# Kernel tuning notes

Measured on AMD Instinct MI355X. Metric: run time of the kernel, lower is better.

Reference implementation:

```python
import jax, jax.numpy as jnp
import numpy as np

# Config (lite version of KimiK2): 2 layers, dim 2048, 16 heads x 128, MLA latent rank 512,
# 4 experts / top-2, SwiGLU inter dim 1024, vocab 32000, batch 2, seq 1024.
DEPTH, DIM, H, HD, R, DFF, E, TOPK, V, B, S = 2, 2048, 16, 128, 512, 1024, 4, 2, 32000, 2, 1024
EPS = 1e-6


def rmsnorm(x, w):
    var = jnp.mean(jnp.square(x), axis=-1, keepdims=True)
    return x * jax.lax.rsqrt(var + EPS) * w


def setup_inputs() -> dict:
    key = jax.random.key(0)
    ks = jax.random.split(key, 16)
    sd = 0.02
    d = {
        'x_tokens': jax.random.randint(ks[0], (B, S), 0, V),
        'emb': jax.random.normal(ks[1], (V, DIM), jnp.float32) * sd,
        'embed_norm_w': jnp.ones((DIM,), jnp.float32),
        # per-layer stacked params (leading axis DEPTH)
        'norm_w': jnp.ones((DEPTH, DIM), jnp.float32),
        'Wq': jax.random.normal(ks[2], (DEPTH, DIM, H * HD), jnp.float32) * sd,
        'Wdkv': jax.random.normal(ks[3], (DEPTH, DIM, R), jnp.float32) * sd,
        'Wuk': jax.random.normal(ks[4], (DEPTH, R, H * HD), jnp.float32) * sd,
        'Wuv': jax.random.normal(ks[5], (DEPTH, R, H * HD), jnp.float32) * sd,
        'Wo': jax.random.normal(ks[6], (DEPTH, H * HD, DIM), jnp.float32) * sd,
        'Wg': jax.random.normal(ks[7], (DEPTH, DIM, E), jnp.float32) * sd,
        'W1': jax.random.normal(ks[8], (DEPTH, E, DIM, DFF), jnp.float32) * sd,
        'W3': jax.random.normal(ks[9], (DEPTH, E, DIM, DFF), jnp.float32) * sd,
        'W2': jax.random.normal(ks[10], (DEPTH, E, DFF, DIM), jnp.float32) * sd,
        'head_norm_w': jnp.ones((DIM,), jnp.float32),
        'head_W': jax.random.normal(ks[11], (DIM, V), jnp.float32) * sd,
        'head_b': jnp.zeros((V,), jnp.float32),
    }
    return d


def mla(x, Wq, Wdkv, Wuk, Wuv, Wo):
    # Multi-head latent attention: queries from x, K/V from a low-rank latent c.
    Bq, Sq, _ = x.shape
    q = (x @ Wq).reshape(Bq, Sq, H, HD)
    c = x @ Wdkv                                   # [B,S,R] compressed KV latent
    k = (c @ Wuk).reshape(Bq, Sq, H, HD)
    v = (c @ Wuv).reshape(Bq, Sq, H, HD)
    scores = jnp.einsum('bqhd,bkhd->bhqk', q, k) / jnp.sqrt(jnp.float32(HD))
    a = jax.nn.softmax(scores, axis=-1)            # block never passes a mask -> full attention
    o = jnp.einsum('bhqk,bkhd->bqhd', a, v).reshape(Bq, Sq, H * HD)
    return o @ Wo


def moe(x, Wg, W1, W3, W2):
    # x: [B,S,D] -> flatten tokens. Dense-over-experts (E=4) with top-k masked gates.
    Bq, Sq, Dq = x.shape
    xt = x.reshape(Bq * Sq, Dq)                    # [T,D]
    gate = jax.nn.softmax(xt @ Wg, axis=-1)        # [T,E]
    topv, topi = jax.lax.top_k(gate, TOPK)
    topv = topv / jnp.sum(topv, axis=-1, keepdims=True)
    gw = jnp.zeros_like(gate).at[jnp.arange(xt.shape[0])[:, None], topi].set(topv)  # [T,E]
    h = jnp.einsum('td,edf->etf', xt, W1)
    g = jnp.einsum('td,edf->etf', xt, W3)
    eo = jnp.einsum('etf,efd->etd', jax.nn.silu(h) * g, W2)
    out = jnp.einsum('etd,te->td', eo, gw)
    return out.reshape(Bq, Sq, Dq)


def reference(x_tokens, emb, embed_norm_w, norm_w, Wq, Wdkv, Wuk, Wuv, Wo, Wg, W1, W3, W2, head_norm_w, head_W, head_b):
    h = emb[x_tokens]
    h = rmsnorm(h, embed_norm_w)

    def layer(h, p):
        nw, wq, wdkv, wuk, wuv, wo, wg, w1, w3, w2 = p
        h = h + mla(rmsnorm(h, nw), wq, wdkv, wuk, wuv, wo)
        # NOTE: same norm weight reused pre-MoE, as in the torch module
        h = h + moe(rmsnorm(h, nw), wg, w1, w3, w2)
        return h, None

    h, _ = jax.lax.scan(layer, h, (norm_w, Wq, Wdkv, Wuk, Wuv, Wo, Wg, W1, W3, W2))
    return rmsnorm(h, head_norm_w) @ head_W + head_b
```

## Files before the change

### kernel.cpp

```cpp
#include <hip/hip_runtime.h>
#include <hip/hip_bf16.h>

typedef __hip_bfloat16 bf16;
typedef __bf16 bf16x8 __attribute__((ext_vector_type(8)));
typedef float f32x4 __attribute__((ext_vector_type(4)));
typedef unsigned short u16;
typedef unsigned int u32;

static constexpr int TOKS = 2048, DM = 2048, RL = 512, DF = 1024, SQ = 1024, NV = 32000;
static constexpr long PL_X  = (long)TOKS * DM;
static constexpr long PL_C  = (long)TOKS * RL;
static constexpr long PL_VT = 2l * 16 * 128 * 1024;
static constexpr long M4 = 4l * 1024 * 1024;
static constexpr long M2 = 2l * 1024 * 1024;

__device__ __forceinline__ float b2f(bf16 x){ return __bfloat162float(x); }
__device__ __forceinline__ bf16  f2b(float x){ return __float2bfloat16(x); }
__device__ __forceinline__ void split1(float x, u16& h, u16& l){
  bf16 hb = f2b(x);
  float r = x - b2f(hb);
  bf16 lb = f2b(r);
  h = *(u16*)&hb; l = *(u16*)&lb;
}

__device__ __forceinline__ float block_red(float v, int op){
  __shared__ float red[4];
  const int lane = threadIdx.x & 63, wv = threadIdx.x >> 6;
  #pragma unroll
  for (int off = 32; off > 0; off >>= 1){
    float o = __shfl_down(v, off, 64);
    v = op ? fmaxf(v, o) : v + o;
  }
  __syncthreads();
  if (lane == 0) red[wv] = v;
  __syncthreads();
  float r = red[0];
  #pragma unroll
  for (int i = 1; i < 4; ++i) r = op ? fmaxf(r, red[i]) : r + red[i];
  return r;
}

__global__ __launch_bounds__(256)
void embed_norm_k(const int* __restrict__ toks, const float* __restrict__ emb,
                  const float* __restrict__ w, float* __restrict__ h){
  const int t = blockIdx.x;
  const long tok = toks[t];
  const int base = threadIdx.x * 8;
  const float* ep = emb + tok * (long)DM + base;
  float4 va = *(const float4*)ep, vb = *(const float4*)(ep + 4);
  float v[8] = {va.x, va.y, va.z, va.w, vb.x, vb.y, vb.z, vb.w};
  float ss = 0.f;
  #pragma unroll
  for (int i = 0; i < 8; ++i) ss += v[i]*v[i];
  ss = block_red(ss, 0);
  const float inv = rsqrtf(ss / DM + 1e-6f);
  float4 wa = *(const float4*)(w + base), wb4 = *(const float4*)(w + base + 4);
  float wv[8] = {wa.x, wa.y, wa.z, wa.w, wb4.x, wb4.y, wb4.z, wb4.w};
  float* hp = h + (long)t * DM + base;
  #pragma unroll
  for (int i = 0; i < 8; ++i) hp[i] = v[i] * inv * wv[i];
}

__global__ __launch_bounds__(256)
void rmsnorm_planes_k(const float* __restrict__ h, const float* __restrict__ w,
                      u16* __restrict__ hi, u16* __restrict__ lo){
  const int t = blockIdx.x;
  const int base = threadIdx.x * 8;
  const float* hp = h + (long)t * DM + base;
  float4 va = *(const float4*)hp, vb = *(const float4*)(hp + 4);
  float v[8] = {va.x, va.y, va.z, va.w, vb.x, vb.y, vb.z, vb.w};
  float ss = 0.f;
  #pragma unroll
  for (int i = 0; i < 8; ++i) ss += v[i]*v[i];
  ss = block_red(ss, 0);
  const float inv = rsqrtf(ss / DM + 1e-6f);
  float4 wa = *(const float4*)(w + base), wb4 = *(const float4*)(w + base + 4);
  float wv[8] = {wa.x, wa.y, wa.z, wa.w, wb4.x, wb4.y, wb4.z, wb4.w};
  u16 hvv[8], lvv[8];
  #pragma unroll
  for (int i = 0; i < 8; ++i) split1(v[i] * inv * wv[i], hvv[i], lvv[i]);
  *(int4*)(hi + (long)t * DM + base) = *(const int4*)hvv;
  *(int4*)(lo + (long)t * DM + base) = *(const int4*)lvv;
}

__global__ __launch_bounds__(256)
void gate_k(const float* __restrict__ h, const float* __restrict__ nw,
            const float* __restrict__ Wg, float* __restrict__ gw){
  const int t = blockIdx.x;
  const int base = threadIdx.x * 8;
  const float* hp = h + (long)t * DM + base;
  float4 va = *(const float4*)hp, vb = *(const float4*)(hp + 4);
  float v[8] = {va.x, va.y, va.z, va.w, vb.x, vb.y, vb.z, vb.w};
  float ss = 0.f;
  #pragma unroll
  for (int i = 0; i < 8; ++i) ss += v[i]*v[i];
  ss = block_red(ss, 0);
  const float inv = rsqrtf(ss / DM + 1e-6f);
  float a[4] = {0.f, 0.f, 0.f, 0.f};
  #pragma unroll
  for (int i = 0; i < 8; ++i){
    const float xv = v[i] * inv * nw[base + i];
    #pragma unroll
    for (int e = 0; e < 4; ++e) a[e] += xv * Wg[(base + i)*4 + e];
  }
  #pragma unroll
  for (int e = 0; e < 4; ++e) a[e] = block_red(a[e], 0);
  if (threadIdx.x == 0){
    int i1 = 0;
    for (int e = 1; e < 4; ++e) if (a[e] > a[i1]) i1 = e;
    int i2 = -1;
    for (int e = 0; e < 4; ++e){ if (e == i1) continue; if (i2 < 0 || a[e] > a[i2]) i2 = e; }
    float g[4];
    const float m = fmaxf(fmaxf(a[0], a[1]), fmaxf(a[2], a[3]));
    float s = 0.f;
    for (int e = 0; e < 4; ++e){ g[e] = __expf(a[e] - m); s += g[e]; }
    for (int e = 0; e < 4; ++e) g[e] /= s;
    const float ns = g[i1] + g[i2];
    float* op = gw + (long)t * 4;
    op[0] = 0.f; op[1] = 0.f; op[2] = 0.f; op[3] = 0.f;
    op[i1] = g[i1] / ns; op[i2] = g[i2] / ns;
  }
}

__global__ __launch_bounds__(256)
void softmax_pack_k(float* __restrict__ pf){
  const long row = blockIdx.x;
  const float* pr = pf + row * SQ;
  const int base = threadIdx.x * 4;
  float4 v4 = *(const float4*)(pr + base);
  float v[4] = {v4.x, v4.y, v4.z, v4.w};
  float m = fmaxf(fmaxf(v[0], v[1]), fmaxf(v[2], v[3]));
  m = block_red(m, 1);
  float s = 0.f;
  #pragma unroll
  for (int i = 0; i < 4; ++i){ v[i] = __expf(v[i] - m); s += v[i]; }
  s = block_red(s, 0);
  const float inv = 1.f / s;
  u16 hv[4], lv[4];
  #pragma unroll
  for (int i = 0; i < 4; ++i) split1(v[i] * inv, hv[i], lv[i]);
  u16* out = (u16*)pf + row * 2048;
  *(int2*)(out + base) = *(const int2*)hv;
  *(int2*)(out + 1024 + base) = *(const int2*)lv;
}

__global__ __launch_bounds__(256)
void swiglu_pack_k(float* __restrict__ h1, const float* __restrict__ h3){
  const int t = threadIdx.x;
  const long r = (long)blockIdx.x * 2 + (t >> 7);
  const int col = (t & 127) * 8;
  const float* p1 = h1 + r * 1024 + col;
  const float* p3 = h3 + r * 1024 + col;
  float4 a0 = *(const float4*)p1, a1 = *(const float4*)(p1 + 4);
  float4 b0 = *(const float4*)p3, b1 = *(const float4*)(p3 + 4);
  float a[8] = {a0.x, a0.y, a0.z, a0.w, a1.x, a1.y, a1.z, a1.w};
  float b[8] = {b0.x, b0.y, b0.z, b0.w, b1.x, b1.y, b1.z, b1.w};
  u16 hv[8], lv[8];
  #pragma unroll
  for (int j = 0; j < 8; ++j){
    const float y = (a[j] / (1.f + __expf(-a[j]))) * b[j];
    split1(y, hv[j], lv[j]);
  }
  __syncthreads();
  u16* out = (u16*)h1 + r * 2048;
  *(int4*)(out + col) = *(const int4*)hv;
  *(int4*)(out + 1024 + col) = *(const int4*)lv;
}

__global__ __launch_bounds__(256)
void swiglu_bk(bf16* __restrict__ h1, const bf16* __restrict__ h3){
  const long i = ((long)blockIdx.x * 256 + threadIdx.x) * 8;
  union { int4 i4; bf16 b[8]; } x, y;
  x.i4 = *(const int4*)(h1 + i);
  y.i4 = *(const int4*)(h3 + i);
  #pragma unroll
  for (int j = 0; j < 8; ++j){
    const float a = b2f(x.b[j]);
    const float b = b2f(y.b[j]);
    x.b[j] = f2b((a / (1.f + __expf(-a))) * b);
  }
  *(int4*)(h1 + i) = x.i4;
}

__global__ __launch_bounds__(256)
void tsplit_k(const float* __restrict__ in, long inz, int ldin,
              u16* __restrict__ oh, u16* __restrict__ ol, long outz, int ldout, int ntx){
  __shared__ u16 lh[64][72], ll[64][72];
  const int z = blockIdx.z;
  in += (long)z * inz; oh += (long)z * outz; ol += (long)z * outz;
  const int bx = blockIdx.x % ntx, by = blockIdx.x / ntx;
  const int k0 = by * 64, n0 = bx * 64;
  const int t = threadIdx.x;
  {
    const int r = t >> 2, cb = (t & 3) * 16;
    const float* ip = in + (long)(k0 + r) * ldin + n0 + cb;
    #pragma unroll
    for (int i = 0; i < 16; i += 4){
      float4 v = *(const float4*)(ip + i);
      float a[4] = {v.x, v.y, v.z, v.w};
      #pragma unroll
      for (int j = 0; j < 4; ++j){
        u16 hv, lv; split1(a[j], hv, lv);
        lh[r][cb + i + j] = hv; ll[r][cb + i + j] = lv;
      }
    }
  }
  __syncthreads();
  {
    const int n = t >> 2, kb = (t & 3) * 16;
    u16 hv[16], lv[16];
    #pragma unroll
    for (int i = 0; i < 16; ++i){ hv[i] = lh[kb + i][n]; lv[i] = ll[kb + i][n]; }
    u16* po = oh + (long)(n0 + n) * ldout + k0 + kb;
    u16* pl = ol + (long)(n0 + n) * ldout + k0 + kb;
    *(int4*)po = *(const int4*)hv; *(int4*)(po + 8) = *(const int4*)(hv + 8);
    *(int4*)pl = *(const int4*)lv; *(int4*)(pl + 8) = *(const int4*)(lv + 8);
  }
}

__global__ __launch_bounds__(256)
void tconv_k(const float* __restrict__ in, long inz, int ldin,
             bf16* __restrict__ out, long outz, int ldout, int ntx){
  __shared__ u16 lh[64][72];
  const int z = blockIdx.z;
  in += (long)z * inz; out += (long)z * outz;
  const int bx = blockIdx.x % ntx, by = blockIdx.x / ntx;
  const int k0 = by * 64, n0 = bx * 64;
  const int t = threadIdx.x;
  {
    const int r = t >> 2, cb = (t & 3) * 16;
    const float* ip = in + (long)(k0 + r) * ldin + n0 + cb;
    #pragma unroll
    for (int i = 0; i < 16; i += 4){
      float4 v = *(const float4*)(ip + i);
      float a[4] = {v.x, v.y, v.z, v.w};
      #pragma unroll
      for (int j = 0; j < 4; ++j){ bf16 hb = f2b(a[j]); lh[r][cb + i + j] = *(u16*)&hb; }
    }
  }
  __syncthreads();
  {
    const int n = t >> 2, kb = (t & 3) * 16;
    u16 hv[16];
    #pragma unroll
    for (int i = 0; i < 16; ++i) hv[i] = lh[kb + i][n];
    u16* po = (u16*)out + (long)(n0 + n) * ldout + k0 + kb;
    *(int4*)po = *(const int4*)hv; *(int4*)(po + 8) = *(const int4*)(hv + 8);
  }
}

static constexpr int KP = 40;
__device__ __forceinline__ int swz(int row, int col){
  return ((((col >> 3) + (row >> 3)) & 3) << 3) | (col & 7);
}
__device__ __forceinline__ int2 tile_xy(int ny){
  const int nwg = gridDim.x;
  const int wid = blockIdx.x;
  const int q = nwg >> 3, r = nwg & 7;
  const int xcd = wid & 7, pos = wid >> 3;
  const int lid = (xcd < r) ? (xcd*(q+1) + pos) : (r*(q+1) + (xcd - r)*q + pos);
  return make_int2(lid / ny, lid % ny);
}

template<int MT, int OM>
__global__ __launch_bounds__(256)
void gemms_nt(const u16* __restrict__ Ah, const u16* __restrict__ Al, long ab, int lda,
              const u16* __restrict__ Bh, const u16* __restrict__ Bl, long bb, int ldb,
              void* __restrict__ Cv, long cb, int ldc, long cpl,
              int K, float scale, const float* __restrict__ aux, int gst, int ny)
{
  __shared__ __align__(16) u16 ash[MT*32][KP], asl[MT*32][KP];
  __shared__ __align__(16) u16 bsh[128][KP], bsl[128][KP];
  const int z = blockIdx.z;
  Ah += (long)z * ab; Al += (long)z * ab;
  Bh += (long)z * bb; Bl += (long)z * bb;
  const int2 tt = tile_xy(ny);
  const int m0 = tt.y * (MT*32), n0 = tt.x * 128;
  const int tid = threadIdx.x, lane = tid & 63, wid = tid >> 6;
  const int wr = (wid >> 1) * (MT*16), wc = (wid & 1) * 64;
  const int fr = lane & 15, fk = (lane >> 4) * 8;

  f32x4 acc[MT][4] = {};

  for (int k0 = 0; k0 < K; k0 += 32){
    __syncthreads();
    #pragma unroll
    for (int p = 0; p < MT/2; ++p){
      const int idx = p * 256 + tid;
      const int r = idx >> 2, c = (idx & 3) * 8;
      const long go = (long)(m0 + r) * lda + k0 + c;
      *(int4*)&ash[r][swz(r, c)] = *(const int4*)(Ah + go);
      *(int4*)&asl[r][swz(r, c)] = *(const int4*)(Al + go);
    }
    #pragma unroll
    for (int p = 0; p < 2; ++p){
      const int idx = p * 256 + tid;
      const int r = idx >> 2, c = (idx & 3) * 8;
      const long go = (long)(n0 + r) * ldb + k0 + c;
      *(int4*)&bsh[r][swz(r, c)] = *(const int4*)(Bh + go);
      *(int4*)&bsl[r][swz(r, c)] = *(const int4*)(Bl + go);
    }
    __syncthreads();
    bf16x8 ahf[MT], alf[MT], bhf[4], blf[4];
    #pragma unroll
    for (int mi = 0; mi < MT; ++mi){
      const int rr = wr + mi * 16 + fr;
      const int sc = swz(rr, fk);
      ahf[mi] = *(const bf16x8*)&ash[rr][sc];
      alf[mi] = *(const bf16x8*)&asl[rr][sc];
    }
    #pragma unroll
    for (int ni = 0; ni < 4; ++ni){
      const int rr = wc + ni * 16 + fr;
      const int sc = swz(rr, fk);
      bhf[ni] = *(const bf16x8*)&bsh[rr][sc];
      blf[ni] = *(const bf16x8*)&bsl[rr][sc];
    }
    #pragma unroll
    for (int mi = 0; mi < MT; ++mi)
      #pragma unroll
      for (int ni = 0; ni < 4; ++ni){
        acc[mi][ni] = __builtin_amdgcn_mfma_f32_16x16x32_bf16(ahf[mi], bhf[ni], acc[mi][ni], 0, 0, 0);
        acc[mi][ni] = __builtin_amdgcn_mfma_f32_16x16x32_bf16(ahf[mi], blf[ni], acc[mi][ni], 0, 0, 0);
        acc[mi][ni] = __builtin_amdgcn_mfma_f32_16x16x32_bf16(alf[mi], bhf[ni], acc[mi][ni], 0, 0, 0);
      }
  }

  const int crow = (lane >> 4) * 4, ccol = lane & 15;
  #pragma unroll
  for (int mi = 0; mi < MT; ++mi){
    #pragma unroll
    for (int ni = 0; ni < 4; ++ni){
      const int gm0 = m0 + wr + mi * 16 + crow;
      const int gn = n0 + wc + ni * 16 + ccol;
      if (OM == 5){
        u16 hv[4], lv[4];
        #pragma unroll
        for (int j = 0; j < 4; ++j) split1(acc[mi][ni][j], hv[j], lv[j]);
        const long off = (((long)(gm0 >> 10) * 16 + (gn >> 7)) * 128 + (gn & 127)) * 1024 + (gm0 & 1023);
        u16* vt = (u16*)Cv;
        *(int2*)(vt + off) = *(const int2*)hv;
        *(int2*)(vt + cpl + off) = *(const int2*)lv;
      } else {
        #pragma unroll
        for (int j = 0; j < 4; ++j){
          const long off = (long)z * cb + (long)(gm0 + j) * ldc + gn;
          const float v = acc[mi][ni][j];
          if (OM == 0)      ((float*)Cv)[off] = v * scale;
          else if (OM == 1) ((float*)Cv)[off] += v;
          else if (OM == 3) ((float*)Cv)[off] += aux[(long)(gm0 + j) * gst] * v;
          else { u16 hv, lv; split1(v, hv, lv); ((u16*)Cv)[off] = hv; ((u16*)Cv)[off + cpl] = lv; }
        }
      }
    }
  }
}

template<int MT, int OM>
__global__ __launch_bounds__(256)
void gemmb_nt(const bf16* __restrict__ A, long ab, int lda,
              const bf16* __restrict__ B, long bb, int ldb,
              void* __restrict__ Cv, long cb, int ldc,
              int K, const float* __restrict__ aux, int gst, int ny)
{
  __shared__ __align__(16) bf16 a_lds[MT*32][KP];
  __shared__ __align__(16) bf16 b_lds[128][KP];
  const int z = blockIdx.z;
  A += (long)z * ab; B += (long)z * bb;
  const int2 tt = tile_xy(ny);
  const int m0 = tt.y * (MT*32), n0 = tt.x * 128;
  const int tid = threadIdx.x, lane = tid & 63, wid = tid >> 6;
  const int wr = (wid >> 1) * (MT*16), wc = (wid & 1) * 64;
  const int fr = lane & 15, fk = (lane >> 4) * 8;

  f32x4 acc[MT][4] = {};

  for (int k0 = 0; k0 < K; k0 += 32){
    __syncthreads();
    #pragma unroll
    for (int p = 0; p < MT/2; ++p){
      const int idx = p * 256 + tid;
      const int r = idx >> 2, c = (idx & 3) * 8;
      *(int4*)&a_lds[r][swz(r, c)] = *(const int4*)(A + (long)(m0 + r) * lda + k0 + c);
    }
    #pragma unroll
    for (int p = 0; p < 2; ++p){
      const int idx = p * 256 + tid;
      const int r = idx >> 2, c = (idx & 3) * 8;
      *(int4*)&b_lds[r][swz(r, c)] = *(const int4*)(B + (long)(n0 + r) * ldb + k0 + c);
    }
    __syncthreads();
    bf16x8 af[MT], bfv[4];
    #pragma unroll
    for (int mi = 0; mi < MT; ++mi){
      const int rr = wr + mi * 16 + fr;
      af[mi] = *(const bf16x8*)&a_lds[rr][swz(rr, fk)];
    }
    #pragma unroll
    for (int ni = 0; ni < 4; ++ni){
      const int rr = wc + ni * 16 + fr;
      bfv[ni] = *(const bf16x8*)&b_lds[rr][swz(rr, fk)];
    }
    #pragma unroll
    for (int mi = 0; mi < MT; ++mi)
      #pragma unroll
      for (int ni = 0; ni < 4; ++ni)
        acc[mi][ni] = __builtin_amdgcn_mfma_f32_16x16x32_bf16(af[mi], bfv[ni], acc[mi][ni], 0, 0, 0);
  }

  const int crow = (lane >> 4) * 4, ccol = lane & 15;
  #pragma unroll
  for (int mi = 0; mi < MT; ++mi){
    #pragma unroll
    for (int ni = 0; ni < 4; ++ni){
      const int gm0 = m0 + wr + mi * 16 + crow;
      const int gn = n0 + wc + ni * 16 + ccol;
      #pragma unroll
      for (int j = 0; j < 4; ++j){
        const long off = (long)z * cb + (long)(gm0 + j) * ldc + gn;
        const float v = acc[mi][ni][j];
        if (OM == 0)      ((bf16*)Cv)[off] = f2b(v);
        else if (OM == 2) ((float*)Cv)[off] = v + aux[gn];
        else              atomicAdd(&((float*)Cv)[off], aux[(long)(gm0 + j) * gst + z] * v);
      }
    }
  }
}

extern "C" void kernel_launch(void* const* d_in, const int* in_sizes, int n_in,
                              void* d_out, int out_size, void* d_ws, size_t ws_size,
                              hipStream_t stream)
{
  (void)in_sizes; (void)n_in; (void)out_size; (void)ws_size;
  const int*   toks = (const int*)d_in[0];
  const float* emb  = (const float*)d_in[1];
  const float* enw  = (const float*)d_in[2];
  const float* nw   = (const float*)d_in[3];
  const float* Wq   = (const float*)d_in[4];
  const float* Wdkv = (const float*)d_in[5];
  const float* Wuk  = (const float*)d_in[6];
  const float* Wuv  = (const float*)d_in[7];
  const float* Wo   = (const float*)d_in[8];
  const float* Wg   = (const float*)d_in[9];
  const float* W1   = (const float*)d_in[10];
  const float* W3   = (const float*)d_in[11];
  const float* W2   = (const float*)d_in[12];
  const float* hnw  = (const float*)d_in[13];
  const float* hW   = (const float*)d_in[14];
  const float* hb   = (const float*)d_in[15];

  const size_t MB = 1ull << 20;
  char* ws = (char*)d_ws;
  float* h    = (float*)(ws);
  float* gw   = (float*)(ws + 16*MB);
  u16*   xph  = (u16*)(ws + 17*MB);
  u16*   wpl  = (u16*)(ws + 33*MB);
  u16*   qph  = (u16*)(ws + 49*MB);
  u16*   cph  = (u16*)(ws + 65*MB);
  u16*   kph  = (u16*)(ws + 69*MB);
  u16*   vtp  = (u16*)(ws + 85*MB);
  u16*   oph  = (u16*)(ws + 101*MB);
  float* pf   = (float*)(ws + 17*MB);
  float* h1f  = (float*)(ws + 49*MB);
  float* h3f  = (float*)(ws + 65*MB);
  bf16*  wT   = (bf16*)(ws + 33*MB);
  bf16*  h1b  = (bf16*)(ws + 49*MB);
  bf16*  h3b  = (bf16*)(ws + 65*MB);
  bf16*  whT  = (bf16*)(ws + 33*MB);

  const float qscale = 0.08838834764831845f;

  embed_norm_k<<<TOKS, 256, 0, stream>>>(toks, emb, enw, h);

  for (int l = 0; l < 2; ++l){
    const float* nwl = nw + (long)l * DM;
    rmsnorm_planes_k<<<TOKS, 256, 0, stream>>>(h, nwl, xph, xph + PL_X);

    tsplit_k<<<1024, 256, 0, stream>>>(Wq + (long)l*DM*DM, 0, DM, wpl, wpl + M4, 0, DM, 32);
    gemms_nt<4,4><<<dim3(256,1,1), 256, 0, stream>>>(xph, xph + PL_X, 0, DM, wpl, wpl + M4, 0, DM,
        qph, 0, DM, PL_X, DM, 1.f, nullptr, 0, 16);
    tsplit_k<<<256, 256, 0, stream>>>(Wdkv + (long)l*DM*RL, 0, RL, wpl, wpl + M2, 0, DM, 8);
    gemms_nt<4,4><<<dim3(64,1,1), 256, 0, stream>>>(xph, xph + PL_X, 0, DM, wpl, wpl + M2, 0, DM,
        cph, 0, RL, PL_C, DM, 1.f, nullptr, 0, 16);
    tsplit_k<<<256, 256, 0, stream>>>(Wuk + (long)l*RL*DM, 0, DM, wpl, wpl + M2, 0, RL, 32);
    gemms_nt<4,4><<<dim3(256,1,1), 256, 0, stream>>>(cph, cph + PL_C, 0, RL, wpl, wpl + M2, 0, RL,
        kph, 0, DM, PL_X, RL, 1.f, nullptr, 0, 16);
    tsplit_k<<<256, 256, 0, stream>>>(Wuv + (long)l*RL*DM, 0, DM, wpl, wpl + M2, 0, RL, 32);
    gemms_nt<4,5><<<dim3(256,1,1), 256, 0, stream>>>(cph, cph + PL_C, 0, RL, wpl, wpl + M2, 0, RL,
        vtp, 0, 0, PL_VT, RL, 1.f, nullptr, 0, 16);

    for (int b = 0; b < 2; ++b){
      for (int hg = 0; hg < 2; ++hg){
        const long qo = (long)b*SQ*DM + hg*1024;
        gemms_nt<4,0><<<dim3(64,1,8), 256, 0, stream>>>(qph + qo, qph + PL_X + qo, 128, DM,
            kph + qo, kph + PL_X + qo, 128, DM,
            pf, (long)SQ*SQ, SQ, 0, 128, qscale, nullptr, 0, 8);
        softmax_pack_k<<<8*SQ, 256, 0, stream>>>(pf);
        const long vo = ((long)b*16 + hg*8) * 128 * 1024;
        gemms_nt<2,4><<<dim3(16,1,8), 256, 0, stream>>>((const u16*)pf, (const u16*)pf + 1024,
            1024l*2048, 2048,
            vtp + vo, vtp + PL_VT + vo, 128l*1024, 1024,
            oph + (long)b*SQ*DM + hg*1024, 128, DM, PL_X, SQ, 1.f, nullptr, 0, 16);
      }
    }

    tsplit_k<<<1024, 256, 0, stream>>>(Wo + (long)l*DM*DM, 0, DM, wpl, wpl + M4, 0, DM, 32);
    gemms_nt<4,1><<<dim3(256,1,1), 256, 0, stream>>>(oph, oph + PL_X, 0, DM, wpl, wpl + M4, 0, DM,
        h, 0, DM, 0, DM, 1.f, nullptr, 0, 16);

    gate_k<<<TOKS, 256, 0, stream>>>(h, nwl, Wg + (long)l*DM*4, gw);
    rmsnorm_planes_k<<<TOKS, 256, 0, stream>>>(h, nwl, xph, xph + PL_X);

    if (l == 0){
      for (int p2 = 0; p2 < 2; ++p2){
        const long wo13 = ((long)l*4 + p2*2) * (long)DM * DF;
        tsplit_k<<<dim3(512,1,2), 256, 0, stream>>>(W1 + wo13, (long)DM*DF, DF, wpl, wpl + M4, M2, DM, 16);
        gemms_nt<2,0><<<dim3(256,1,2), 256, 0, stream>>>(xph, xph + PL_X, 0, DM, wpl, wpl + M4, M2, DM,
            h1f, (long)TOKS*DF, DF, 0, DM, 1.f, nullptr, 0, 32);
        tsplit_k<<<dim3(512,1,2), 256, 0, stream>>>(W3 + wo13, (long)DM*DF, DF, wpl, wpl + M4, M2, DM, 16);
        gemms_nt<2,0><<<dim3(256,1,2), 256, 0, stream>>>(xph, xph + PL_X, 0, DM, wpl, wpl + M4, M2, DM,
            h3f, (long)TOKS*DF, DF, 0, DM, 1.f, nullptr, 0, 32);
        swiglu_pack_k<<<2048, 256, 0, stream>>>(h1f, h3f);
        tsplit_k<<<dim3(512,1,2), 256, 0, stream>>>(W2 + ((long)l*4 + p2*2)*(long)DF*DM, (long)DF*DM, DM,
            wpl, wpl + M4, M2, DF, 32);
        for (int ei = 0; ei < 2; ++ei){
          gemms_nt<4,3><<<dim3(256,1,1), 256, 0, stream>>>(
              (const u16*)h1f + (long)ei*TOKS*2048, (const u16*)h1f + (long)ei*TOKS*2048 + 1024,
              0, 2048, wpl + (long)ei*M2, wpl + M4 + (long)ei*M2, 0, DF,
              h, 0, DM, 0, DF, 1.f, gw + p2*2 + ei, 4, 16);
        }
      }
    } else {
      tconv_k<<<dim3(512,1,4), 256, 0, stream>>>(W1 + (long)l*4*DM*DF, (long)DM*DF, DF, wT, M2, DM, 16);
      gemmb_nt<2,0><<<dim3(256,1,4), 256, 0, stream>>>((const bf16*)xph, 0, DM, wT, M2, DM,
          h1b, (long)TOKS*DF, DF, DM, nullptr, 0, 32);
      tconv_k<<<dim3(512,1,4), 256, 0, stream>>>(W3 + (long)l*4*DM*DF, (long)DM*DF, DF, wT, M2, DM, 16);
      gemmb_nt<2,0><<<dim3(256,1,4), 256, 0, stream>>>((const bf16*)xph, 0, DM, wT, M2, DM,
          h3b, (long)TOKS*DF, DF, DM, nullptr, 0, 32);
      swiglu_bk<<<4096, 256, 0, stream>>>(h1b, h3b);
      tconv_k<<<dim3(512,1,4), 256, 0, stream>>>(W2 + (long)l*4*DF*DM, (long)DF*DM, DM, wT, M2, DF, 32);
      gemmb_nt<4,3><<<dim3(256,1,4), 256, 0, stream>>>(h1b, (long)TOKS*DF, DF, wT, M2, DF,
          h, 0, DM, DF, gw, 4, 16);
    }
  }

  rmsnorm_planes_k<<<TOKS, 256, 0, stream>>>(h, hnw, xph, xph + PL_X);
  for (int half = 0; half < 2; ++half){
    tconv_k<<<8000, 256, 0, stream>>>(hW + half*16000, 0, NV, whT, 0, DM, 250);
    gemmb_nt<4,2><<<dim3(2000,1,1), 256, 0, stream>>>((const bf16*)xph, 0, DM, whT, 0, DM,
        (float*)d_out + half*16000, 0, NV, DM, hb + half*16000, 0, 16);
  }
}
```

Measured before the change: 2.661 ms.

## Stage GEMM tiles via direct global-to-LDS loads with new swizzle

Replaces the register-staged global loads plus LDS stores in both split-bf16 and plain bf16 GEMM kernels with __builtin_amdgcn_global_load_lds, which writes 16-byte chunks straight into shared memory. The LDS tiles lose their row padding and use a new XOR-style swizzle (swz2), applied on the global-address side so the fragment reads avoid bank conflicts. The aim is to cut VGPR traffic and LDS write instructions in the staging path. In exchange the kernel relies on the direct-to-LDS instruction's layout semantics, which it can get wrong, and the loop remains single-buffered with no added overlap.

Result: faster. 2.521 ms (-5.3%).

```diff
diff --git a/kernel.cpp b/kernel.cpp
--- a/kernel.cpp
+++ b/kernel.cpp
@@ -6,6 +6,8 @@
 typedef float f32x4 __attribute__((ext_vector_type(4)));
 typedef unsigned short u16;
 typedef unsigned int u32;
+typedef __attribute__((address_space(1))) const void* gptr_t;
+typedef __attribute__((address_space(3))) void* lptr_t;
 
 static constexpr int TOKS = 2048, DM = 2048, RL = 512, DF = 1024, SQ = 1024, NV = 32000;
 static constexpr long PL_X  = (long)TOKS * DM;
@@ -249,9 +251,8 @@
   }
 }
 
-static constexpr int KP = 40;
-__device__ __forceinline__ int swz(int row, int col){
-  return ((((col >> 3) + (row >> 3)) & 3) << 3) | (col & 7);
+__device__ __forceinline__ int swz2(int r, int c){
+  return ((((c >> 3) + (r >> 1)) & 3) << 3) | (c & 7);
 }
 __device__ __forceinline__ int2 tile_xy(int ny){
   const int nwg = gridDim.x;
@@ -262,6 +263,14 @@
   return make_int2(lid / ny, lid % ny);
 }
 
+__device__ __forceinline__ void stage_issue(const u16* src, int ld, int rbase, int k0,
+                                            u16* lp, int sub, int lane){
+  const int r = sub * 16 + (lane >> 2);
+  const int cs = ((lane & 3) - (r >> 1)) & 3;
+  const u16* g = src + (long)(rbase + r) * ld + k0 + cs * 8;
+  __builtin_amdgcn_global_load_lds((gptr_t)g, (lptr_t)(lp + sub * 512), 16, 0, 0);
+}
+
 template<int MT, int OM>
 __global__ __launch_bounds__(256)
 void gemms_nt(const u16* __restrict__ Ah, const u16* __restrict__ Al, long ab, int lda,
@@ -269,50 +278,43 @@
               void* __restrict__ Cv, long cb, int ldc, long cpl,
               int K, float scale, const float* __restrict__ aux, int gst, int ny)
 {
-  __shared__ __align__(16) u16 ash[MT*32][KP], asl[MT*32][KP];
-  __shared__ __align__(16) u16 bsh[128][KP], bsl[128][KP];
+  __shared__ __align__(16) u16 ash[MT*32][32], asl[MT*32][32];
+  __shared__ __align__(16) u16 bsh[128][32], bsl[128][32];
   const int z = blockIdx.z;
   Ah += (long)z * ab; Al += (long)z * ab;
   Bh += (long)z * bb; Bl += (long)z * bb;
   const int2 tt = tile_xy(ny);
   const int m0 = tt.y * (MT*32), n0 = tt.x * 128;
-  const int tid = threadIdx.x, lane = tid & 63, wid = tid >> 6;
-  const int wr = (wid >> 1) * (MT*16), wc = (wid & 1) * 64;
+  const int tid = threadIdx.x, lane = tid & 63, wv = tid >> 6;
+  const int wr = (wv >> 1) * (MT*16), wc = (wv & 1) * 64;
   const int fr = lane & 15, fk = (lane >> 4) * 8;
 
   f32x4 acc[MT][4] = {};
+  constexpr int AI = MT * 2;
 
   for (int k0 = 0; k0 < K; k0 += 32){
     __syncthreads();
     #pragma unroll
-    for (int p = 0; p < MT/2; ++p){
-      const int idx = p * 256 + tid;
-      const int r = idx >> 2, c = (idx & 3) * 8;
-      const long go = (long)(m0 + r) * lda + k0 + c;
-      *(int4*)&ash[r][swz(r, c)] = *(const int4*)(Ah + go);
-      *(int4*)&asl[r][swz(r, c)] = *(const int4*)(Al + go);
-    }
-    #pragma unroll
-    for (int p = 0; p < 2; ++p){
-      const int idx = p * 256 + tid;
-      const int r = idx >> 2, c = (idx & 3) * 8;
-      const long go = (long)(n0 + r) * ldb + k0 + c;
-      *(int4*)&bsh[r][swz(r, c)] = *(const int4*)(Bh + go);
-      *(int4*)&bsl[r][swz(r, c)] = *(const int4*)(Bl + go);
+    for (int ii = 0; ii < 2*AI + 16; ++ii){
+      if ((ii & 3) != wv) continue;
+      if (ii < AI)            stage_issue(Ah, lda, m0, k0, &ash[0][0], ii, lane);
+      else if (ii < 2*AI)     stage_issue(Al, lda, m0, k0, &asl[0][0], ii - AI, lane);
+      else if (ii < 2*AI + 8) stage_issue(Bh, ldb, n0, k0, &bsh[0][0], ii - 2*AI, lane);
+      else                    stage_issue(Bl, ldb, n0, k0, &bsl[0][0], ii - 2*AI - 8, lane);
     }
     __syncthreads();
     bf16x8 ahf[MT], alf[MT], bhf[4], blf[4];
     #pragma unroll
     for (int mi = 0; mi < MT; ++mi){
       const int rr = wr + mi * 16 + fr;
-      const int sc = swz(rr, fk);
+      const int sc = swz2(rr, fk);
       ahf[mi] = *(const bf16x8*)&ash[rr][sc];
       alf[mi] = *(const bf16x8*)&asl[rr][sc];
     }
     #pragma unroll
     for (int ni = 0; ni < 4; ++ni){
       const int rr = wc + ni * 16 + fr;
-      const int sc = swz(rr, fk);
+      const int sc = swz2(rr, fk);
       bhf[ni] = *(const bf16x8*)&bsh[rr][sc];
       blf[ni] = *(const bf16x8*)&bsl[rr][sc];
     }
@@ -363,43 +365,38 @@
               void* __restrict__ Cv, long cb, int ldc,
               int K, const float* __restrict__ aux, int gst, int ny)
 {
-  __shared__ __align__(16) bf16 a_lds[MT*32][KP];
-  __shared__ __align__(16) bf16 b_lds[128][KP];
+  __shared__ __align__(16) u16 a_lds[MT*32][32];
+  __shared__ __align__(16) u16 b_lds[128][32];
   const int z = blockIdx.z;
   A += (long)z * ab; B += (long)z * bb;
   const int2 tt = tile_xy(ny);
   const int m0 = tt.y * (MT*32), n0 = tt.x * 128;
-  const int tid = threadIdx.x, lane = tid & 63, wid = tid >> 6;
-  const int wr = (wid >> 1) * (MT*16), wc = (wid & 1) * 64;
+  const int tid = threadIdx.x, lane = tid & 63, wv = tid >> 6;
+  const int wr = (wv >> 1) * (MT*16), wc = (wv & 1) * 64;
   const int fr = lane & 15, fk = (lane >> 4) * 8;
 
   f32x4 acc[MT][4] = {};
+  constexpr int AI = MT * 2;
 
   for (int k0 = 0; k0 < K; k0 += 32){
     __syncthreads();
     #pragma unroll
-    for (int p = 0; p < MT/2; ++p){
-      const int idx = p * 256 + tid;
-      const int r = idx >> 2, c = (idx & 3) * 8;
-      *(int4*)&a_lds[r][swz(r, c)] = *(const int4*)(A + (long)(m0 + r) * lda + k0 + c);
-    }
-    #pragma unroll
-    for (int p = 0; p < 2; ++p){
-      const int idx = p * 256 + tid;
-      const int r = idx >> 2, c = (idx & 3) * 8;
-      *(int4*)&b_lds[r][swz(r, c)] = *(const int4*)(B + (long)(n0 + r) * ldb + k0 + c);
+    for (int ii = 0; ii < AI + 8; ++ii){
+      if ((ii & 3) != wv) continue;
+      if (ii < AI) stage_issue((const u16*)A, lda, m0, k0, &a_lds[0][0], ii, lane);
+      else         stage_issue((const u16*)B, ldb, n0, k0, &b_lds[0][0], ii - AI, lane);
     }
     __syncthreads();
     bf16x8 af[MT], bfv[4];
     #pragma unroll
     for (int mi = 0; mi < MT; ++mi){
       const int rr = wr + mi * 16 + fr;
-      af[mi] = *(const bf16x8*)&a_lds[rr][swz(rr, fk)];
+      af[mi] = *(const bf16x8*)&a_lds[rr][swz2(rr, fk)];
     }
     #pragma unroll
     for (int ni = 0; ni < 4; ++ni){
       const int rr = wc + ni * 16 + fr;
-      bfv[ni] = *(const bf16x8*)&b_lds[rr][swz(rr, fk)];
+      bfv[ni] = *(const bf16x8*)&b_lds[rr][swz2(rr, fk)];
     }
     #pragma unroll
     for (int mi = 0; mi < MT; ++mi)
```
